# Kernel tuning notes

Measured on AMD Instinct MI355X. Metric: run time of the kernel, lower is better.

Reference implementation:

```python
import jax, jax.numpy as jnp
import numpy as np

B, N, C = 1, 4096, 1024
H = 16
HD = C // H  # head_dim = 64
SCALE = HD ** -0.5


def setup_inputs() -> dict:
    key = jax.random.key(0)
    k1, k2, k3, k4, k5 = jax.random.split(key, 5)
    x1 = jax.random.normal(k1, (B, N, C), dtype=jnp.float32)
    x2 = jax.random.normal(k2, (B, N, C), dtype=jnp.float32)
    # qkv: Linear(dim, 2*all_head_dim), bias=False. Stored as (in, out) for x @ W.
    W_qkv = jax.random.normal(k3, (C, 2 * H * HD), dtype=jnp.float32) * (C ** -0.5)
    # proj: Linear(all_head_dim, dim) with bias
    W_proj = jax.random.normal(k4, (H * HD, C), dtype=jnp.float32) * ((H * HD) ** -0.5)
    b_proj = jax.random.normal(k5, (C,), dtype=jnp.float32) * 0.01
    return {"x1": x1, "x2": x2, "W_qkv": W_qkv, "W_proj": W_proj, "b_proj": b_proj}


def reference(x1, x2, W_qkv, W_proj, b_proj):
    b, n, c = x1.shape
    # qk projection: (B,N,2*H*HD) -> (2,B,H,N,HD)
    qkv = (x1 @ W_qkv).reshape(b, n, 2, H, HD).transpose(2, 0, 3, 1, 4)
    q, k = qkv[0], qkv[1]  # (B,H,N,HD)
    # V2: reshape (N,1,H,HD) then permute -> (1,H,N,HD); valid since B==1
    v = x2.reshape(n, 1, H, HD).transpose(1, 2, 0, 3)
    attn = jax.nn.softmax(jnp.einsum('bhnd,bhmd->bhnm', q * SCALE, k), axis=-1)
    out = jnp.einsum('bhnm,bhmd->bhnd', attn, v)  # broadcasts v over batch
    out = out.transpose(0, 2, 1, 3).reshape(b, n, H * HD)
    return out @ W_proj + b_proj
```

## Files before the change

### kernel.cpp

```cpp
#include <hip/hip_runtime.h>

typedef unsigned short u16;
typedef unsigned int u32;

#define HNUM 16
#define NSEQ 4096
#define CDIM 1024
#define SCALE 0.125f
#define LOG2E 1.4426950408889634f

using bf16x8 = __attribute__((ext_vector_type(8))) __bf16;
using f32x4  = __attribute__((ext_vector_type(4))) float;

__device__ __forceinline__ u16 f2bf(float f) {
  union { float f; u32 u; } v; v.f = f;
  u32 u = v.u;
  return (u16)((u + 0x7fffu + ((u >> 16) & 1u)) >> 16);
}
__device__ __forceinline__ float fexp2(float x) { return __builtin_amdgcn_exp2f(x); }

__device__ __forceinline__ f32x4 mfma16(bf16x8 a, bf16x8 b, f32x4 c) {
  return __builtin_amdgcn_mfma_f32_16x16x32_bf16(a, b, c, 0, 0, 0);
}

__device__ __forceinline__ u32 pack2(float a, float b) {
  union { float f; u32 u; } A, B;
  A.f = a; B.f = b;
  return __builtin_amdgcn_perm(B.u + 0x8000u, A.u + 0x8000u, 0x07060302u);
}

__device__ __forceinline__ void g2l16(const void* g, void* l) {
  __builtin_amdgcn_global_load_lds(
      (const __attribute__((address_space(1))) unsigned int*)(unsigned long long)g,
      (__attribute__((address_space(3))) unsigned int*)(unsigned int)(unsigned long long)l,
      16, 0, 0);
}

__global__ __launch_bounds__(256) void cvt_k(const float* __restrict__ in,
                                             u16* __restrict__ out) {
  const int i = (blockIdx.x * 256 + threadIdx.x) * 8;
  const float4 f0 = *(const float4*)(in + i);
  const float4 f1 = *(const float4*)(in + i + 4);
  u32 d[4] = {pack2(f0.x, f0.y), pack2(f0.z, f0.w),
              pack2(f1.x, f1.y), pack2(f1.z, f1.w)};
  *(bf16x8*)(out + i) = *(bf16x8*)d;
}

__global__ __launch_bounds__(256) void cvtT_k(const float* __restrict__ in,
                                              u16* __restrict__ out, int R, int C,
                                              int scaleRows, float scale) {
  __shared__ u16 t[64][65];
  const int tid = threadIdx.x;
  const int r0 = blockIdx.y * 64, c0 = blockIdx.x * 64;
  const int tr = tid >> 2, tc = (tid & 3) * 16;
  const float s = (c0 < scaleRows) ? scale : 1.0f;
  const float* src = in + (r0 + tr) * C + c0 + tc;
#pragma unroll
  for (int i = 0; i < 16; ++i) t[tr][tc + i] = f2bf(src[i] * s);
  __syncthreads();
  u16* dst = out + (c0 + tr) * R + r0 + tc;
#pragma unroll
  for (int i = 0; i < 16; ++i) dst[i] = t[tc + i][tr];
}

__global__ __launch_bounds__(256) void gemm1_k(const u16* __restrict__ A,
                                               const u16* __restrict__ Bt,
                                               u16* __restrict__ C,
                                               int M, int N, int K) {
  __shared__ __align__(16) u16 As[128 * 64];
  __shared__ __align__(16) u16 Bs[128 * 64];
  const int tid = threadIdx.x;
  const int wave = tid >> 6, lane = tid & 63;
  const int quad = lane >> 4, l16 = lane & 15;
  const int m0 = blockIdx.y * 128, n0 = blockIdx.x * 128;
  const int wm = (wave >> 1) * 64, wn = (wave & 1) * 64;
  const int lrow = lane >> 3, lc8 = (lane & 7) * 8;

  f32x4 acc[4][4] = {};
  for (int k0 = 0; k0 < K; k0 += 64) {
#pragma unroll
    for (int c = 0; c < 4; ++c) {
      const int cw = wave * 4 + c;
      g2l16(A  + (m0 + cw * 8 + lrow) * K + k0 + lc8, (char*)As + cw * 1024);
      g2l16(Bt + (n0 + cw * 8 + lrow) * K + k0 + lc8, (char*)Bs + cw * 1024);
    }
    __syncthreads();
#pragma unroll
    for (int ks = 0; ks < 2; ++ks) {
      bf16x8 a[4], b[4];
#pragma unroll
      for (int mt = 0; mt < 4; ++mt)
        a[mt] = *(const bf16x8*)(As + (wm + mt * 16 + l16) * 64 + ks * 32 + quad * 8);
#pragma unroll
      for (int nt = 0; nt < 4; ++nt)
        b[nt] = *(const bf16x8*)(Bs + (wn + nt * 16 + l16) * 64 + ks * 32 + quad * 8);
#pragma unroll
      for (int mt = 0; mt < 4; ++mt)
#pragma unroll
        for (int nt = 0; nt < 4; ++nt)
          acc[mt][nt] = mfma16(a[mt], b[nt], acc[mt][nt]);
    }
    __syncthreads();
  }
#pragma unroll
  for (int mt = 0; mt < 4; ++mt)
#pragma unroll
    for (int nt = 0; nt < 4; ++nt)
#pragma unroll
      for (int r = 0; r < 4; ++r)
        C[(m0 + wm + mt * 16 + quad * 4 + r) * N + n0 + wn + nt * 16 + l16] =
            f2bf(acc[mt][nt][r]);
}

__global__ __launch_bounds__(256) void gemm2_k(const u16* __restrict__ A,
                                               const u16* __restrict__ Bt,
                                               float* __restrict__ C,
                                               const float* __restrict__ bias,
                                               int M, int N, int K) {
  __shared__ __align__(16) u16 As[128 * 64];
  __shared__ __align__(16) u16 Bs[128 * 64];
  const int tid = threadIdx.x;
  const int wave = tid >> 6, lane = tid & 63;
  const int quad = lane >> 4, l16 = lane & 15;
  const int m0 = blockIdx.y * 128, n0 = blockIdx.x * 128;
  const int wm = (wave >> 1) * 64, wn = (wave & 1) * 64;
  const int lrow = lane >> 3, lc8 = (lane & 7) * 8;

  f32x4 acc[4][4] = {};
  for (int k0 = 0; k0 < K; k0 += 64) {
#pragma unroll
    for (int c = 0; c < 4; ++c) {
      const int cw = wave * 4 + c;
      g2l16(A  + (m0 + cw * 8 + lrow) * K + k0 + lc8, (char*)As + cw * 1024);
      g2l16(Bt + (n0 + cw * 8 + lrow) * K + k0 + lc8, (char*)Bs + cw * 1024);
    }
    __syncthreads();
#pragma unroll
    for (int ks = 0; ks < 2; ++ks) {
      bf16x8 a[4], b[4];
#pragma unroll
      for (int mt = 0; mt < 4; ++mt)
        a[mt] = *(const bf16x8*)(As + (wm + mt * 16 + l16) * 64 + ks * 32 + quad * 8);
#pragma unroll
      for (int nt = 0; nt < 4; ++nt)
        b[nt] = *(const bf16x8*)(Bs + (wn + nt * 16 + l16) * 64 + ks * 32 + quad * 8);
#pragma unroll
      for (int mt = 0; mt < 4; ++mt)
#pragma unroll
        for (int nt = 0; nt < 4; ++nt)
          acc[mt][nt] = mfma16(a[mt], b[nt], acc[mt][nt]);
    }
    __syncthreads();
  }
#pragma unroll
  for (int mt = 0; mt < 4; ++mt)
#pragma unroll
    for (int nt = 0; nt < 4; ++nt)
#pragma unroll
      for (int r = 0; r < 4; ++r) {
        const int col = n0 + wn + nt * 16 + l16;
        C[(m0 + wm + mt * 16 + quad * 4 + r) * N + col] = acc[mt][nt][r] + bias[col];
      }
}

__global__ __launch_bounds__(128) void attn_k(const u16* __restrict__ QK,
                                              const u16* __restrict__ Vt,
                                              u16* __restrict__ O) {
  __shared__ __align__(16) u16 Ks[2][64 * 64];
  __shared__ __align__(16) u16 Vs[2][64 * 64];
  __shared__ __align__(16) u16 Ps[2][32 * 64];
  const int tid = threadIdx.x;
  const int wave = tid >> 6, lane = tid & 63;
  const int quad = lane >> 4, l16 = lane & 15;
  const int head = blockIdx.y;
  const int qb = blockIdx.x * 64 + wave * 32;
  const int lrow = lane >> 3;
  const int lc8 = ((lane & 7) ^ lrow) * 8;
  const int swz = (quad ^ (l16 & 7)) * 8;

  const u16* kp[4];
  const u16* vp[4];
#pragma unroll
  for (int c = 0; c < 4; ++c) {
    const int row = (wave * 4 + c) * 8 + lrow;
    kp[c] = QK + row * 2048 + CDIM + head * 64 + lc8;
    vp[c] = Vt + (head * 64 + row) * NSEQ + lc8;
  }

  bf16x8 qf[2][2];
#pragma unroll
  for (int mt = 0; mt < 2; ++mt)
#pragma unroll
    for (int ks = 0; ks < 2; ++ks)
      qf[mt][ks] = *(const bf16x8*)(QK + (qb + mt * 16 + l16) * 2048 + head * 64 +
                                    ks * 32 + quad * 8);

  f32x4 o[2][4] = {};
  float lsum[2] = {};
  u16* Pw = Ps[wave];

#pragma unroll
  for (int c = 0; c < 4; ++c) {
    const int cw = wave * 4 + c;
    g2l16(kp[c], (char*)Ks[0] + cw * 1024);
    g2l16(vp[c], (char*)Vs[0] + cw * 1024);
    kp[c] += 64 * 2048;
    vp[c] += 64;
  }

  for (int kt = 0; kt < NSEQ / 64; ++kt) {
    const int cur = kt & 1;
    __syncthreads();

    if (kt < NSEQ / 64 - 1) {
#pragma unroll
      for (int c = 0; c < 4; ++c) {
        const int cw = wave * 4 + c;
        g2l16(kp[c], (char*)Ks[1 - cur] + cw * 1024);
        g2l16(vp[c], (char*)Vs[1 - cur] + cw * 1024);
        kp[c] += 64 * 2048;
        vp[c] += 64;
      }
    }

    const u16* Kc = Ks[cur];
    const u16* Vc = Vs[cur];

    f32x4 s[2][4] = {};
#pragma unroll
    for (int ks = 0; ks < 2; ++ks)
#pragma unroll
      for (int nt = 0; nt < 4; ++nt) {
        const bf16x8 kf =
            *(const bf16x8*)(Kc + (nt * 16 + l16) * 64 + (swz ^ (ks * 32)));
#pragma unroll
        for (int mt = 0; mt < 2; ++mt)
          s[mt][nt] = mfma16(kf, qf[mt][ks], s[mt][nt]);
      }

#pragma unroll
    for (int mt = 0; mt < 2; ++mt)
#pragma unroll
      for (int nt = 0; nt < 4; ++nt) {
        const float p0 = fexp2(s[mt][nt][0]);
        const float p1 = fexp2(s[mt][nt][1]);
        const float p2 = fexp2(s[mt][nt][2]);
        const float p3 = fexp2(s[mt][nt][3]);
        lsum[mt] += (p0 + p1) + (p2 + p3);
        u32 d01 = pack2(p0, p1), d23 = pack2(p2, p3);
        const int col8 = (nt * 2 + (quad >> 1)) ^ (l16 & 7);
        u32* dst = (u32*)(Pw + (mt * 16 + l16) * 64 + col8 * 8 + (quad & 1) * 4);
        dst[0] = d01; dst[1] = d23;
      }

#pragma unroll
    for (int ks = 0; ks < 2; ++ks) {
      bf16x8 pf[2];
#pragma unroll
      for (int mt = 0; mt < 2; ++mt)
        pf[mt] = *(const bf16x8*)(Pw + (mt * 16 + l16) * 64 + (swz ^ (ks * 32)));
#pragma unroll
      for (int dt = 0; dt < 4; ++dt) {
        const bf16x8 vf =
            *(const bf16x8*)(Vc + (dt * 16 + l16) * 64 + (swz ^ (ks * 32)));
#pragma unroll
        for (int mt = 0; mt < 2; ++mt)
          o[mt][dt] = mfma16(pf[mt], vf, o[mt][dt]);
      }
    }
  }

  float linv[2];
#pragma unroll
  for (int mt = 0; mt < 2; ++mt) {
    float v = lsum[mt];
    v += __shfl_xor(v, 16, 64);
    v += __shfl_xor(v, 32, 64);
    linv[mt] = 1.0f / v;
  }
#pragma unroll
  for (int mt = 0; mt < 2; ++mt)
#pragma unroll
    for (int r = 0; r < 4; ++r) {
      const float lv = __shfl(linv[mt], (lane & 48) | (quad * 4 + r), 64);
#pragma unroll
      for (int dt = 0; dt < 4; ++dt)
        O[(qb + mt * 16 + quad * 4 + r) * CDIM + head * 64 + dt * 16 + l16] =
            f2bf(o[mt][dt][r] * lv);
    }
}

extern "C" void kernel_launch(void* const* d_in, const int* in_sizes, int n_in,
                              void* d_out, int out_size, void* d_ws, size_t ws_size,
                              hipStream_t stream) {
  const float* x1    = (const float*)d_in[0];
  const float* x2    = (const float*)d_in[1];
  const float* Wqkv  = (const float*)d_in[2];
  const float* Wproj = (const float*)d_in[3];
  const float* bproj = (const float*)d_in[4];
  float* out = (float*)d_out;

  char* ws = (char*)d_ws;
  u16* QK  = (u16*)(ws);
  u16* Vt  = (u16*)(ws + 16u * 1024 * 1024);
  u16* Obf = (u16*)(ws + 24u * 1024 * 1024);
  u16* WpT = (u16*)(ws + 32u * 1024 * 1024);
  u16* WqT = (u16*)(ws + 34u * 1024 * 1024);
  u16* x1b = (u16*)(ws + 38u * 1024 * 1024);

  const float cfac = SCALE * LOG2E;

  cvt_k<<<dim3(4096 * 1024 / 2048), 256, 0, stream>>>(x1, x1b);
  cvtT_k<<<dim3(2048 / 64, 1024 / 64), 256, 0, stream>>>(Wqkv, WqT, 1024, 2048,
                                                         1024, cfac);
  cvtT_k<<<dim3(1024 / 64, 1024 / 64), 256, 0, stream>>>(Wproj, WpT, 1024, 1024,
                                                         0, 1.0f);
  cvtT_k<<<dim3(1024 / 64, 4096 / 64), 256, 0, stream>>>(x2, Vt, 4096, 1024,
                                                         0, 1.0f);

  gemm1_k<<<dim3(2048 / 128, 4096 / 128), 256, 0, stream>>>(x1b, WqT, QK,
                                                            4096, 2048, 1024);
  attn_k<<<dim3(4096 / 64, HNUM), 128, 0, stream>>>(QK, Vt, Obf);
  gemm2_k<<<dim3(1024 / 128, 4096 / 128), 256, 0, stream>>>(Obf, WpT, out, bproj,
                                                            4096, 1024, 1024);
}
```

Before: 255.4 us.

## Software-pipeline PV MFMA across iterations and shrink proj GEMM tile to 128x64

In the attention kernel, the P and V fragments are loaded into registers at the end of each KV iteration. The P·V MFMAs for that tile are deferred into the next iteration, after the barrier and the next prefetch issue, so they overlap with the following QK^T and exp work. A final epilogue consumes the last tile. The output-projection GEMM tile goes from 128x128 to 128x64, which doubles its block count (256 to 512) to fill more CUs, at the cost of less operand reuse per block and more register-held fragments in attention.

```diff
diff --git a/kernel.cpp b/kernel.cpp
--- a/kernel.cpp
+++ b/kernel.cpp
@@ -118,34 +118,38 @@
                                                const float* __restrict__ bias,
                                                int M, int N, int K) {
   __shared__ __align__(16) u16 As[128 * 64];
-  __shared__ __align__(16) u16 Bs[128 * 64];
+  __shared__ __align__(16) u16 Bs[64 * 64];
   const int tid = threadIdx.x;
   const int wave = tid >> 6, lane = tid & 63;
   const int quad = lane >> 4, l16 = lane & 15;
-  const int m0 = blockIdx.y * 128, n0 = blockIdx.x * 128;
-  const int wm = (wave >> 1) * 64, wn = (wave & 1) * 64;
+  const int m0 = blockIdx.y * 128, n0 = blockIdx.x * 64;
+  const int wm = wave * 32;
   const int lrow = lane >> 3, lc8 = (lane & 7) * 8;
 
-  f32x4 acc[4][4] = {};
+  f32x4 acc[2][4] = {};
   for (int k0 = 0; k0 < K; k0 += 64) {
 #pragma unroll
     for (int c = 0; c < 4; ++c) {
       const int cw = wave * 4 + c;
-      g2l16(A  + (m0 + cw * 8 + lrow) * K + k0 + lc8, (char*)As + cw * 1024);
+      g2l16(A + (m0 + cw * 8 + lrow) * K + k0 + lc8, (char*)As + cw * 1024);
+    }
+#pragma unroll
+    for (int c = 0; c < 2; ++c) {
+      const int cw = wave * 2 + c;
       g2l16(Bt + (n0 + cw * 8 + lrow) * K + k0 + lc8, (char*)Bs + cw * 1024);
     }
     __syncthreads();
 #pragma unroll
     for (int ks = 0; ks < 2; ++ks) {
-      bf16x8 a[4], b[4];
-#pragma unroll
-      for (int mt = 0; mt < 4; ++mt)
+      bf16x8 a[2], b[4];
+#pragma unroll
+      for (int mt = 0; mt < 2; ++mt)
         a[mt] = *(const bf16x8*)(As + (wm + mt * 16 + l16) * 64 + ks * 32 + quad * 8);
 #pragma unroll
       for (int nt = 0; nt < 4; ++nt)
-        b[nt] = *(const bf16x8*)(Bs + (wn + nt * 16 + l16) * 64 + ks * 32 + quad * 8);
-#pragma unroll
-      for (int mt = 0; mt < 4; ++mt)
+        b[nt] = *(const bf16x8*)(Bs + (nt * 16 + l16) * 64 + ks * 32 + quad * 8);
+#pragma unroll
+      for (int mt = 0; mt < 2; ++mt)
 #pragma unroll
         for (int nt = 0; nt < 4; ++nt)
           acc[mt][nt] = mfma16(a[mt], b[nt], acc[mt][nt]);
@@ -153,12 +157,12 @@
     __syncthreads();
   }
 #pragma unroll
-  for (int mt = 0; mt < 4; ++mt)
+  for (int mt = 0; mt < 2; ++mt)
 #pragma unroll
     for (int nt = 0; nt < 4; ++nt)
 #pragma unroll
       for (int r = 0; r < 4; ++r) {
-        const int col = n0 + wn + nt * 16 + l16;
+        const int col = n0 + nt * 16 + l16;
         C[(m0 + wm + mt * 16 + quad * 4 + r) * N + col] = acc[mt][nt][r] + bias[col];
       }
 }
@@ -197,6 +201,8 @@
 
   f32x4 o[2][4] = {};
   float lsum[2] = {};
+  bf16x8 pfr[2][2];
+  bf16x8 vfr[2][4];
   u16* Pw = Ps[wave];
 
 #pragma unroll
@@ -211,6 +217,16 @@
   for (int kt = 0; kt < NSEQ / 64; ++kt) {
     const int cur = kt & 1;
     __syncthreads();
+
+    if (kt > 0) {
+#pragma unroll
+      for (int ks = 0; ks < 2; ++ks)
+#pragma unroll
+        for (int dt = 0; dt < 4; ++dt)
+#pragma unroll
+          for (int mt = 0; mt < 2; ++mt)
+            o[mt][dt] = mfma16(pfr[mt][ks], vfr[ks][dt], o[mt][dt]);
+    }
 
     if (kt < NSEQ / 64 - 1) {
 #pragma unroll
@@ -254,21 +270,25 @@
       }
 
 #pragma unroll
-    for (int ks = 0; ks < 2; ++ks) {
-      bf16x8 pf[2];
+    for (int mt = 0; mt < 2; ++mt)
+#pragma unroll
+      for (int ks = 0; ks < 2; ++ks)
+        pfr[mt][ks] = *(const bf16x8*)(Pw + (mt * 16 + l16) * 64 + (swz ^ (ks * 32)));
+#pragma unroll
+    for (int ks = 0; ks < 2; ++ks)
+#pragma unroll
+      for (int dt = 0; dt < 4; ++dt)
+        vfr[ks][dt] =
+            *(const bf16x8*)(Vc + (dt * 16 + l16) * 64 + (swz ^ (ks * 32)));
+  }
+
+#pragma unroll
+  for (int ks = 0; ks < 2; ++ks)
+#pragma unroll
+    for (int dt = 0; dt < 4; ++dt)
 #pragma unroll
       for (int mt = 0; mt < 2; ++mt)
-        pf[mt] = *(const bf16x8*)(Pw + (mt * 16 + l16) * 64 + (swz ^ (ks * 32)));
-#pragma unroll
-      for (int dt = 0; dt < 4; ++dt) {
-        const bf16x8 vf =
-            *(const bf16x8*)(Vc + (dt * 16 + l16) * 64 + (swz ^ (ks * 32)));
-#pragma unroll
-        for (int mt = 0; mt < 2; ++mt)
-          o[mt][dt] = mfma16(pf[mt], vf, o[mt][dt]);
-      }
-    }
-  }
+        o[mt][dt] = mfma16(pfr[mt][ks], vfr[ks][dt], o[mt][dt]);
 
   float linv[2];
 #pragma unroll
@@ -321,6 +341,6 @@
   gemm1_k<<<dim3(2048 / 128, 4096 / 128), 256, 0, stream>>>(x1b, WqT, QK,
                                                             4096, 2048, 1024);
   attn_k<<<dim3(4096 / 64, HNUM), 128, 0, stream>>>(QK, Vt, Obf);
-  gemm2_k<<<dim3(1024 / 128, 4096 / 128), 256, 0, stream>>>(Obf, WpT, out, bproj,
-                                                            4096, 1024, 1024);
-}
+  gemm2_k<<<dim3(1024 / 64, 4096 / 128), 256, 0, stream>>>(Obf, WpT, out, bproj,
+                                                           4096, 1024, 1024);
+}
```

Result: faster. 249.6 us (-2.3%).
